# Performance work log

Hardware: AMD Instinct MI355X
Metric: run time of the kernel (lower is better)

The kernel has to match this reference:

```python
import jax, jax.numpy as jnp
import numpy as np

B, L, D_IN, D_MODEL, D_STATE, N_LAYERS = 16, 2048, 64, 512, 16, 4
LN_EPS = 1e-5


def setup_inputs() -> dict:
    key = jax.random.key(0)
    ks = jax.random.split(key, 16)
    s = 0.02
    x = jax.random.normal(ks[0], (B, L, D_IN), jnp.float32)
    W_in0 = jax.random.normal(ks[1], (D_IN, D_MODEL), jnp.float32) * s
    b_in0 = jnp.zeros((D_MODEL,), jnp.float32)
    W_in = jax.random.normal(ks[2], (N_LAYERS - 1, D_MODEL, D_MODEL), jnp.float32) * s
    b_in = jnp.zeros((N_LAYERS - 1, D_MODEL), jnp.float32)
    # S4D-style init: A_log = log(1..N) per channel
    A_log = jnp.broadcast_to(jnp.log(jnp.arange(1, D_STATE + 1, dtype=jnp.float32)), (N_LAYERS, D_MODEL, D_STATE)).copy()
    D_skip = jnp.ones((N_LAYERS, D_MODEL), jnp.float32)
    W_dt = jax.random.normal(ks[3], (N_LAYERS, D_MODEL, D_MODEL), jnp.float32) * s
    b_dt = jnp.full((N_LAYERS, D_MODEL), -4.0, jnp.float32)  # small initial dt
    W_B = jax.random.normal(ks[4], (N_LAYERS, D_MODEL, D_STATE), jnp.float32) * s
    W_C = jax.random.normal(ks[5], (N_LAYERS, D_MODEL, D_STATE), jnp.float32) * s
    ln_g = jnp.ones((D_MODEL,), jnp.float32)
    ln_b = jnp.zeros((D_MODEL,), jnp.float32)
    head_w = jax.random.normal(ks[6], (D_MODEL, 1), jnp.float32) * s
    head_b = jnp.zeros((1,), jnp.float32)
    return {"x": x, "W_in0": W_in0, "b_in0": b_in0, "W_in": W_in, "b_in": b_in,
            "A_log": A_log, "D_skip": D_skip, "W_dt": W_dt, "b_dt": b_dt,
            "W_B": W_B, "W_C": W_C, "ln_g": ln_g, "ln_b": ln_b,
            "head_w": head_w, "head_b": head_b}


def _mamba_layer(x, W_in_l, b_in_l, A_log_l, D_l, W_dt_l, b_dt_l, W_B_l, W_C_l):
    # x: (B, L, d_in) -> y: (B, L, D_MODEL)
    u = x @ W_in_l + b_in_l                    # (B, L, D)
    dt = jax.nn.softplus(u @ W_dt_l + b_dt_l)  # (B, L, D)
    Bm = u @ W_B_l                             # (B, L, N)
    Cm = u @ W_C_l                             # (B, L, N)
    A = -jnp.exp(A_log_l)                      # (D, N)

    def step(h, inp):
        dt_t, u_t, B_t, C_t = inp              # (B,D),(B,D),(B,N),(B,N)
        dA = jnp.exp(dt_t[..., None] * A)      # (B, D, N)
        h = dA * h + (dt_t * u_t)[..., None] * B_t[:, None, :]
        y_t = jnp.einsum('bdn,bn->bd', h, C_t)
        return h, y_t

    h0 = jnp.zeros((u.shape[0], u.shape[2], A.shape[1]), u.dtype)
    xs = (jnp.swapaxes(dt, 0, 1), jnp.swapaxes(u, 0, 1),
          jnp.swapaxes(Bm, 0, 1), jnp.swapaxes(Cm, 0, 1))
    _, ys = jax.lax.scan(step, h0, xs)         # ys: (L, B, D)
    return jnp.swapaxes(ys, 0, 1) + u * D_l


def reference(x, W_in0, b_in0, W_in, b_in, A_log, D_skip, W_dt, b_dt, W_B, W_C, ln_g, ln_b, head_w, head_b):
    h = x
    for i in range(N_LAYERS):
        Wi = W_in0 if i == 0 else W_in[i - 1]
        bi = b_in0 if i == 0 else b_in[i - 1]
        h = _mamba_layer(h, Wi, bi, A_log[i], D_skip[i], W_dt[i], b_dt[i], W_B[i], W_C[i])
    # LayerNorm over d_model
    mu = jnp.mean(h, axis=-1, keepdims=True)
    var = jnp.mean(jnp.square(h - mu), axis=-1, keepdims=True)
    h = (h - mu) * jax.lax.rsqrt(var + LN_EPS) * ln_g + ln_b
    return h[:, -1, :] @ head_w + head_b       # (B, 1)
```

## Files before the change

kernel.cpp:

```cpp
#include <hip/hip_runtime.h>
#include <hip/hip_bf16.h>
#include <cstdint>
#include <cstddef>

#define B_SZ    16
#define L_SZ    2048
#define DIN     64
#define DMODEL  512
#define DSTATE  16
#define NLAYERS 4
#define LN_EPS  1e-5f
#define NC      32
#define TCH     (L_SZ / NC)
#define NFUSED  (2 * DMODEL)

typedef __bf16 bf16x8 __attribute__((ext_vector_type(8)));
typedef float  f32x4  __attribute__((ext_vector_type(4)));
typedef unsigned short u16;
typedef unsigned int   u32;

__device__ __forceinline__ u16 f2bf(float f) {
    u32 u = __builtin_bit_cast(u32, f);
    u += 0x7fffu + ((u >> 16) & 1u);
    return (u16)(u >> 16);
}
__device__ __forceinline__ float bf2f(u16 v) {
    u32 u = ((u32)v) << 16;
    return __builtin_bit_cast(float, u);
}

__device__ __forceinline__ void pow16(float q, float* a_) {
    float q2 = q * q, q4 = q2 * q2, q8 = q4 * q4;
    a_[0] = q;        a_[1] = q2;       a_[2] = q2 * q;   a_[3] = q4;
    a_[4] = q4 * q;   a_[5] = q4 * q2;  a_[6] = a_[5] * q; a_[7] = q8;
    a_[8] = q8 * q;   a_[9] = q8 * q2;  a_[10] = a_[9] * q; a_[11] = q8 * q4;
    a_[12] = a_[11] * q; a_[13] = a_[11] * q2; a_[14] = a_[13] * q; a_[15] = q8 * q8;
}

#define LOG2E 1.4426950408889634f

__device__ __forceinline__ void gload16(const void* g, void* l) {
    __builtin_amdgcn_global_load_lds(
        (__attribute__((address_space(1))) void*)(g),
        (__attribute__((address_space(3))) void*)(l), 16, 0, 0);
}

template <int K>
__global__ __launch_bounds__(512) void gemm_fused(
    const u16* __restrict__ A, const u16* __restrict__ BT,
    const float* __restrict__ bias, u16* __restrict__ Cu,
    u16* __restrict__ Cdt, int M)
{
    constexpr int BM = 128, BK = 32;
    constexpr int NT = K / BK;
    __shared__ u16 As[2][BM * BK];
    __shared__ u16 Bs[2][BM * BK];

    const int tid = threadIdx.x;
    const int wv = tid >> 6, ln = tid & 63;
    const int mb = blockIdx.x & 255, nb = blockIdx.x >> 8;
    const int bm = mb * BM, bn = nb * BM;
    const int wm = (wv >> 1) * 32, wn = (wv & 1) * 64;

    f32x4 acc[2][4];
#pragma unroll
    for (int i = 0; i < 2; ++i)
#pragma unroll
        for (int j = 0; j < 4; ++j) acc[i][j] = (f32x4){0.f, 0.f, 0.f, 0.f};

    const int sm = tid >> 2, ss = tid & 3;
    const int ksrc = (ss ^ ((sm >> 1) & 3)) * 8;
    auto stage = [&](int buf, int k0) {
        gload16(A + (size_t)(bm + sm) * K + k0 + ksrc, &As[buf][(wv * 64) * 8]);
        gload16(BT + (size_t)(bn + sm) * K + k0 + ksrc, &Bs[buf][(wv * 64) * 8]);
    };

    stage(0, 0);
    if (NT > 1) stage(1, BK);

#pragma unroll
    for (int kt = 0; kt < NT; ++kt) {
        if (kt == NT - 1) asm volatile("s_waitcnt vmcnt(0)" ::: "memory");
        else              asm volatile("s_waitcnt vmcnt(2)" ::: "memory");
        __builtin_amdgcn_s_barrier();

        const int buf = kt & 1;
        const int g = ln >> 4, lm = ln & 15;
        bf16x8 af[2], bfr[4];
#pragma unroll
        for (int e = 0; e < 2; ++e) {
            int ml = wm + e * 16 + lm;
            af[e] = *(const bf16x8*)&As[buf][ml * 32 + ((g ^ ((ml >> 1) & 3)) * 8)];
        }
#pragma unroll
        for (int f = 0; f < 4; ++f) {
            int nl = wn + f * 16 + lm;
            bfr[f] = *(const bf16x8*)&Bs[buf][nl * 32 + ((g ^ ((nl >> 1) & 3)) * 8)];
        }
#pragma unroll
        for (int e = 0; e < 2; ++e)
#pragma unroll
            for (int f = 0; f < 4; ++f)
                acc[e][f] = __builtin_amdgcn_mfma_f32_16x16x32_bf16(
                    af[e], bfr[f], acc[e][f], 0, 0, 0);

        asm volatile("s_waitcnt lgkmcnt(0)" ::: "memory");
        __builtin_amdgcn_s_barrier();
        if (kt + 2 < NT) stage(buf, (kt + 2) * BK);
    }

    const int cg = ln >> 4, lc = ln & 15;
    const bool uside = (bn < DMODEL);
#pragma unroll
    for (int e = 0; e < 2; ++e) {
#pragma unroll
        for (int f = 0; f < 4; ++f) {
            int col = bn + wn + f * 16 + lc;
            float bv = bias[col];
#pragma unroll
            for (int r = 0; r < 4; ++r) {
                int row = bm + wm + e * 16 + cg * 4 + r;
                float v = acc[e][f][r] + bv;
                if (uside) {
                    Cu[(size_t)row * DMODEL + col] = f2bf(v);
                } else {
                    v = (v > 20.f) ? v : __logf(1.f + __expf(v));
                    Cdt[(size_t)row * DMODEL + (col - DMODEL)] = f2bf(v);
                }
            }
        }
    }
}

__global__ __launch_bounds__(256) void wtrans(
    const float* __restrict__ W, u16* __restrict__ WT, int K, int N,
    size_t inStride, size_t outStride)
{
    __shared__ float tile[32][33];
    const float* Wm = W + (size_t)blockIdx.z * inStride;
    u16* WTm = WT + (size_t)blockIdx.z * outStride;
    int k0 = blockIdx.x * 32, n0 = blockIdx.y * 32;
    int tx = threadIdx.x & 31, ty = threadIdx.x >> 5;
#pragma unroll
    for (int i = 0; i < 4; ++i)
        tile[ty + 8 * i][tx] = Wm[(size_t)(k0 + ty + 8 * i) * N + n0 + tx];
    __syncthreads();
#pragma unroll
    for (int i = 0; i < 4; ++i)
        WTm[(size_t)(n0 + ty + 8 * i) * K + k0 + tx] = f2bf(tile[tx][ty + 8 * i]);
}

__global__ __launch_bounds__(256) void wcombo(
    const float* __restrict__ Win, const float* __restrict__ Wdt,
    u16* __restrict__ outT, int KD,
    size_t winStride, size_t wdtStride, size_t outStride)
{
    __shared__ float wi[16][516];
    __shared__ float wd[512][16];
    const float* WinL = Win + (size_t)blockIdx.z * winStride;
    const float* WdtL = Wdt + (size_t)blockIdx.z * wdtStride;
    u16* outL = outT + (size_t)blockIdx.z * outStride;
    const int k0 = blockIdx.x * 16, n0 = blockIdx.y * 16;
    const int tid = threadIdx.x;
    for (int i = tid; i < 16 * 128; i += 256) {
        int r = i >> 7, c = i & 127;
        *(float4*)&wi[r][c * 4] =
            *(const float4*)&WinL[(size_t)(k0 + r) * DMODEL + c * 4];
    }
    for (int i = tid; i < 512 * 4; i += 256) {
        int j = i >> 2, c = i & 3;
        *(float4*)&wd[j][c * 4] =
            *(const float4*)&WdtL[(size_t)j * DMODEL + n0 + c * 4];
    }
    __syncthreads();
    const int kk = tid & 15, nn = tid >> 4;
    float acc = 0.f;
#pragma unroll 8
    for (int j = 0; j < 512; ++j)
        acc = fmaf(wi[kk][j], wd[j][nn], acc);
    outL[(size_t)(n0 + nn) * KD + k0 + kk] = f2bf(acc);
}

__global__ __launch_bounds__(256) void biasprep(
    const float* __restrict__ bin, const float* __restrict__ Wdt,
    const float* __restrict__ bdt, float* __restrict__ biascat,
    size_t binStride, size_t wdtStride, size_t bdtStride, size_t outStride)
{
    const float* binL = bin + (size_t)blockIdx.z * binStride;
    const float* WdtL = Wdt + (size_t)blockIdx.z * wdtStride;
    const float* bdtL = bdt + (size_t)blockIdx.z * bdtStride;
    float* outL = biascat + (size_t)blockIdx.z * outStride;
    int idx = blockIdx.x * 256 + threadIdx.x;
    if (idx < DMODEL) { outL[idx] = binL[idx]; return; }
    int n = idx - DMODEL;
    float acc = bdtL[n];
    for (int j = 0; j < DMODEL; ++j)
        acc = fmaf(binL[j], WdtL[(size_t)j * DMODEL + n], acc);
    outL[idx] = acc;
}

__global__ __launch_bounds__(256) void castx(
    const float* __restrict__ x, u16* __restrict__ xb, int n4)
{
    int i = blockIdx.x * 256 + threadIdx.x;
    if (i < n4) {
        float4 v = ((const float4*)x)[i];
        ushort4 o;
        o.x = f2bf(v.x); o.y = f2bf(v.y); o.z = f2bf(v.z); o.w = f2bf(v.w);
        ((ushort4*)xb)[i] = o;
    }
}

__global__ __launch_bounds__(256) void prep_wbc(
    const float* __restrict__ WB, const float* __restrict__ WC,
    u16* __restrict__ WBCT)
{
    int idx = blockIdx.x * 256 + threadIdx.x;
    int l = idx >> 14;
    int r = idx & 16383;
    int n = r >> 9, k = r & 511;
    float v = (n < 16) ? WB[((size_t)l * DMODEL + k) * DSTATE + n]
                       : WC[((size_t)l * DMODEL + k) * DSTATE + (n - 16)];
    WBCT[((size_t)l * 32 + n) * DMODEL + k] = f2bf(v);
}

__global__ __launch_bounds__(256) void gemm_bc_mfma(
    const u16* __restrict__ A, const u16* __restrict__ WBCT,
    float* __restrict__ Bo, float* __restrict__ Co)
{
    const int tid = threadIdx.x;
    const int wv = tid >> 6, ln = tid & 63;
    const int m0 = blockIdx.x * 64 + wv * 16;
    const int g = ln >> 4, lm = ln & 15;

    f32x4 accB = (f32x4){0.f, 0.f, 0.f, 0.f};
    f32x4 accC = (f32x4){0.f, 0.f, 0.f, 0.f};
    const u16* arow = A + (size_t)(m0 + lm) * DMODEL;
    const u16* wb = WBCT + (size_t)lm * DMODEL;
    const u16* wc = WBCT + (size_t)(lm + 16) * DMODEL;
#pragma unroll
    for (int ks = 0; ks < DMODEL / 32; ++ks) {
        int ko = ks * 32 + g * 8;
        bf16x8 a = *(const bf16x8*)&arow[ko];
        bf16x8 b = *(const bf16x8*)&wb[ko];
        bf16x8 c = *(const bf16x8*)&wc[ko];
        accB = __builtin_amdgcn_mfma_f32_16x16x32_bf16(a, b, accB, 0, 0, 0);
        accC = __builtin_amdgcn_mfma_f32_16x16x32_bf16(a, c, accC, 0, 0, 0);
    }
#pragma unroll
    for (int r = 0; r < 4; ++r) {
        int m = m0 + g * 4 + r;
        Bo[(size_t)m * DSTATE + lm] = accB[r];
        Co[(size_t)m * DSTATE + lm] = accC[r];
    }
}

__global__ __launch_bounds__(256) void scan_pass1(
    const u16* __restrict__ u, const u16* __restrict__ dt,
    const float* __restrict__ Bm, const float* __restrict__ A_log,
    float* __restrict__ P, float* __restrict__ S)
{
    const int tid = threadIdx.x;
    const int d = blockIdx.x * 256 + tid;
    const int c = blockIdx.y, b = blockIdx.z;
    __shared__ float Bs[TCH][DSTATE];

    const float* Bsrc = Bm + ((size_t)b * L_SZ + (size_t)c * TCH) * DSTATE;
    for (int i = tid; i < TCH * DSTATE / 4; i += 256)
        ((float4*)Bs)[i] = ((const float4*)Bsrc)[i];

    float Ac[16];
#pragma unroll
    for (int n = 0; n < 16; ++n) Ac[n] = -__expf(A_log[d * DSTATE + n]);
    bool geo = true;
#pragma unroll
    for (int n = 1; n < 16; ++n)
        geo &= fabsf(Ac[n] - (n + 1) * Ac[0]) <= 1e-4f * (n + 1) * fabsf(Ac[0]);
    __syncthreads();

    float s[16];
#pragma unroll
    for (int n = 0; n < 16; ++n) s[n] = 0.f;

    const size_t base = ((size_t)b * L_SZ + (size_t)c * TCH) * DMODEL + d;
    size_t o = (((size_t)b * NC + c) * DMODEL + d) * DSTATE;

    if (geo) {
        const float cK = Ac[0] * LOG2E;
        float qp = 1.f;
#pragma unroll 2
        for (int t = 0; t < TCH; ++t) {
            float dtv = bf2f(dt[base + (size_t)t * DMODEL]);
            float uv  = bf2f(u [base + (size_t)t * DMODEL]);
            float du = dtv * uv;
            float q = exp2f(dtv * cK);
            qp *= q;
            float a_[16];
            pow16(q, a_);
#pragma unroll
            for (int n = 0; n < 16; ++n)
                s[n] = fmaf(a_[n], s[n], du * Bs[t][n]);
        }
        float p_[16];
        pow16(qp, p_);
#pragma unroll
        for (int n = 0; n < 16; ++n) { P[o + n] = p_[n]; S[o + n] = s[n]; }
    } else {
        float p[16];
#pragma unroll
        for (int n = 0; n < 16; ++n) p[n] = 1.f;
#pragma unroll 2
        for (int t = 0; t < TCH; ++t) {
            float dtv = bf2f(dt[base + (size_t)t * DMODEL]);
            float uv  = bf2f(u [base + (size_t)t * DMODEL]);
            float du = dtv * uv;
#pragma unroll
            for (int n = 0; n < 16; ++n) {
                float a = __expf(dtv * Ac[n]);
                p[n] *= a;
                s[n] = fmaf(a, s[n], du * Bs[t][n]);
            }
        }
#pragma unroll
        for (int n = 0; n < 16; ++n) { P[o + n] = p[n]; S[o + n] = s[n]; }
    }
}

__global__ __launch_bounds__(256) void scan_fix(
    const float* __restrict__ P, const float* __restrict__ S,
    float* __restrict__ H0)
{
    const int idx = blockIdx.x * 256 + threadIdx.x;
    const int dn = idx & (DMODEL * DSTATE - 1);
    const int b = idx >> 13;
    float h = 0.f;
#pragma unroll
    for (int c = 0; c < NC; ++c) {
        size_t o = (((size_t)b * NC + c) << 13) + dn;
        H0[o] = h;
        h = fmaf(P[o], h, S[o]);
    }
}

__global__ __launch_bounds__(256) void scan_pass2(
    const u16* __restrict__ u, const u16* __restrict__ dt,
    const float* __restrict__ Bm, const float* __restrict__ Cm,
    const float* __restrict__ A_log, const float* __restrict__ Dskip,
    const float* __restrict__ H0, u16* __restrict__ yb,
    float* __restrict__ ylast)
{
    const int tid = threadIdx.x;
    const int d = blockIdx.x * 256 + tid;
    const int c = blockIdx.y, b = blockIdx.z;
    __shared__ float Bs[TCH][DSTATE];
    __shared__ float Cs[TCH][DSTATE];

    const float* Bsrc = Bm + ((size_t)b * L_SZ + (size_t)c * TCH) * DSTATE;
    const float* Csrc = Cm + ((size_t)b * L_SZ + (size_t)c * TCH) * DSTATE;
    for (int i = tid; i < TCH * DSTATE / 4; i += 256) {
        ((float4*)Bs)[i] = ((const float4*)Bsrc)[i];
        ((float4*)Cs)[i] = ((const float4*)Csrc)[i];
    }

    float Ac[16];
#pragma unroll
    for (int n = 0; n < 16; ++n) Ac[n] = -__expf(A_log[d * DSTATE + n]);
    bool geo = true;
#pragma unroll
    for (int n = 1; n < 16; ++n)
        geo &= fabsf(Ac[n] - (n + 1) * Ac[0]) <= 1e-4f * (n + 1) * fabsf(Ac[0]);
    const float Dk = Dskip[d];

    float h[16];
    size_t ho = (((size_t)b * NC + c) * DMODEL + d) * DSTATE;
#pragma unroll
    for (int n = 0; n < 16; ++n) h[n] = H0[ho + n];
    __syncthreads();

    const size_t base = ((size_t)b * L_SZ + (size_t)c * TCH) * DMODEL + d;

    if (geo) {
        const float cK = Ac[0] * LOG2E;
#pragma unroll 2
        for (int t = 0; t < TCH; ++t) {
            float dtv = bf2f(dt[base + (size_t)t * DMODEL]);
            float uv  = bf2f(u [base + (size_t)t * DMODEL]);
            float du = dtv * uv;
            float q = exp2f(dtv * cK);
            float a_[16];
            pow16(q, a_);
            float yv = 0.f;
#pragma unroll
            for (int n = 0; n < 16; ++n) {
                h[n] = fmaf(a_[n], h[n], du * Bs[t][n]);
                yv = fmaf(h[n], Cs[t][n], yv);
            }
            yv = fmaf(uv, Dk, yv);
            yb[base + (size_t)t * DMODEL] = f2bf(yv);
            if (c == NC - 1 && t == TCH - 1) ylast[(size_t)b * DMODEL + d] = yv;
        }
    } else {
#pragma unroll 2
        for (int t = 0; t < TCH; ++t) {
            float dtv = bf2f(dt[base + (size_t)t * DMODEL]);
            float uv  = bf2f(u [base + (size_t)t * DMODEL]);
            float du = dtv * uv;
            float yv = 0.f;
#pragma unroll
            for (int n = 0; n < 16; ++n) {
                float a = __expf(dtv * Ac[n]);
                h[n] = fmaf(a, h[n], du * Bs[t][n]);
                yv = fmaf(h[n], Cs[t][n], yv);
            }
            yv = fmaf(uv, Dk, yv);
            yb[base + (size_t)t * DMODEL] = f2bf(yv);
            if (c == NC - 1 && t == TCH - 1) ylast[(size_t)b * DMODEL + d] = yv;
        }
    }
}

__global__ __launch_bounds__(256) void ln_head_kernel(
    const float* __restrict__ ylast, const float* __restrict__ g,
    const float* __restrict__ bb, const float* __restrict__ hw,
    const float* __restrict__ hb, float* __restrict__ out)
{
    const int b = blockIdx.x;
    const int tid = threadIdx.x;
    const float* row = ylast + (size_t)b * DMODEL;
    float v0 = row[tid], v1 = row[tid + 256];
    float s = v0 + v1;
    float s2 = v0 * v0 + v1 * v1;
#pragma unroll
    for (int o = 32; o >= 1; o >>= 1) {
        s += __shfl_xor(s, o);
        s2 += __shfl_xor(s2, o);
    }
    __shared__ float red[8];
    const int w = tid >> 6;
    if ((tid & 63) == 0) { red[w] = s; red[4 + w] = s2; }
    __syncthreads();
    s = red[0] + red[1] + red[2] + red[3];
    s2 = red[4] + red[5] + red[6] + red[7];
    float mu = s * (1.f / DMODEL);
    float var = s2 * (1.f / DMODEL) - mu * mu;
    float r = rsqrtf(var + LN_EPS);
    float c = ((v0 - mu) * r * g[tid] + bb[tid]) * hw[tid]
            + ((v1 - mu) * r * g[tid + 256] + bb[tid + 256]) * hw[tid + 256];
#pragma unroll
    for (int o = 32; o >= 1; o >>= 1) c += __shfl_xor(c, o);
    __syncthreads();
    if ((tid & 63) == 0) red[w] = c;
    __syncthreads();
    if (tid == 0) out[b] = red[0] + red[1] + red[2] + red[3] + hb[0];
}

extern "C" void kernel_launch(void* const* d_in, const int* in_sizes, int n_in,
                              void* d_out, int out_size, void* d_ws, size_t ws_size,
                              hipStream_t stream)
{
    const float* x      = (const float*)d_in[0];
    const float* W_in0  = (const float*)d_in[1];
    const float* b_in0  = (const float*)d_in[2];
    const float* W_in   = (const float*)d_in[3];
    const float* b_in   = (const float*)d_in[4];
    const float* A_log  = (const float*)d_in[5];
    const float* D_skip = (const float*)d_in[6];
    const float* W_dt   = (const float*)d_in[7];
    const float* b_dt   = (const float*)d_in[8];
    const float* W_B    = (const float*)d_in[9];
    const float* W_C    = (const float*)d_in[10];
    const float* ln_g   = (const float*)d_in[11];
    const float* ln_b   = (const float*)d_in[12];
    const float* head_w = (const float*)d_in[13];
    const float* head_b = (const float*)d_in[14];
    float* out = (float*)d_out;

    const size_t BLD = (size_t)B_SZ * L_SZ * DMODEL;
    const size_t BLN = (size_t)B_SZ * L_SZ * DSTATE;
    const size_t BCD = (size_t)B_SZ * NC * DMODEL * DSTATE;
    const size_t XBN = (size_t)B_SZ * L_SZ * DIN;

    float* fp = (float*)d_ws;
    float* Bbuf  = fp; fp += BLN;
    float* Cbuf  = fp; fp += BLN;
    float* Pbuf  = fp; fp += BCD;
    float* Sbuf  = fp; fp += BCD;
    float* H0buf = fp; fp += BCD;
    float* ylast = fp; fp += (size_t)B_SZ * DMODEL;
    float* biascat = fp; fp += (size_t)NLAYERS * NFUSED;
    u16* hp = (u16*)fp;
    u16* xb    = hp; hp += XBN;
    u16* ub    = hp; hp += BLD;
    u16* dtb   = hp; hp += BLD;
    u16* ybuf  = hp; hp += BLD;
    u16* BT0   = hp; hp += (size_t)NFUSED * DIN;
    u16* BTcat = hp; hp += (size_t)(NLAYERS - 1) * NFUSED * DMODEL;
    u16* WBCT  = hp; hp += (size_t)NLAYERS * 32 * DMODEL;

    const int M = B_SZ * L_SZ;

    castx<<<(XBN / 4 + 255) / 256, 256, 0, stream>>>(x, xb, XBN / 4);
    prep_wbc<<<(NLAYERS * 32 * DMODEL) / 256, 256, 0, stream>>>(W_B, W_C, WBCT);
    wtrans<<<dim3(DIN / 32, DMODEL / 32, 1), 256, 0, stream>>>(
        W_in0, BT0, DIN, DMODEL, 0, 0);
    wcombo<<<dim3(DIN / 16, DMODEL / 16, 1), 256, 0, stream>>>(
        W_in0, W_dt, BT0 + (size_t)DMODEL * DIN, DIN, 0, 0, 0);
    biasprep<<<dim3(4, 1, 1), 256, 0, stream>>>(
        b_in0, W_dt, b_dt, biascat, 0, 0, 0, 0);
    wtrans<<<dim3(DMODEL / 32, DMODEL / 32, NLAYERS - 1), 256, 0, stream>>>(
        W_in, BTcat, DMODEL, DMODEL,
        (size_t)DMODEL * DMODEL, (size_t)NFUSED * DMODEL);
    wcombo<<<dim3(DMODEL / 16, DMODEL / 16, NLAYERS - 1), 256, 0, stream>>>(
        W_in, W_dt + (size_t)DMODEL * DMODEL,
        BTcat + (size_t)DMODEL * DMODEL, DMODEL,
        (size_t)DMODEL * DMODEL, (size_t)DMODEL * DMODEL,
        (size_t)NFUSED * DMODEL);
    biasprep<<<dim3(4, 1, NLAYERS - 1), 256, 0, stream>>>(
        b_in, W_dt + (size_t)DMODEL * DMODEL, b_dt + DMODEL, biascat + NFUSED,
        DMODEL, (size_t)DMODEL * DMODEL, DMODEL, NFUSED);

    for (int l = 0; l < NLAYERS; ++l) {
        if (l == 0) {
            gemm_fused<DIN><<<(M / 128) * (NFUSED / 128), 512, 0, stream>>>(
                xb, BT0, biascat, ub, dtb, M);
        } else {
            gemm_fused<DMODEL><<<(M / 128) * (NFUSED / 128), 512, 0, stream>>>(
                ybuf, BTcat + (size_t)(l - 1) * NFUSED * DMODEL,
                biascat + (size_t)l * NFUSED, ub, dtb, M);
        }
        gemm_bc_mfma<<<M / 64, 256, 0, stream>>>(
            ub, WBCT + (size_t)l * 32 * DMODEL, Bbuf, Cbuf);
        const float* Al = A_log + (size_t)l * DMODEL * DSTATE;
        scan_pass1<<<dim3(DMODEL / 256, NC, B_SZ), 256, 0, stream>>>(
            ub, dtb, Bbuf, Al, Pbuf, Sbuf);
        scan_fix<<<(B_SZ * DMODEL * DSTATE) / 256, 256, 0, stream>>>(
            Pbuf, Sbuf, H0buf);
        scan_pass2<<<dim3(DMODEL / 256, NC, B_SZ), 256, 0, stream>>>(
            ub, dtb, Bbuf, Cbuf, Al, D_skip + (size_t)l * DMODEL,
            H0buf, ybuf, ylast);
    }

    ln_head_kernel<<<B_SZ, 256, 0, stream>>>(ylast, ln_g, ln_b, head_w, head_b, out);
}
```

Baseline: 691.7 us.

## Deepen GEMM LDS pipeline to four stages and store compact chunk decay

The fused GEMM moves from two to four LDS buffers with a three-tile prefetch distance. This removes the second barrier and lgkmcnt wait in each k-step, and it raises wave priority around the MFMA block. Separately, scan_pass1 on the geometric-A path writes one scalar chunk decay per channel instead of 16 powers. scan_fix rebuilds each power by repeated squaring, which cuts P-buffer write and read traffic. In exchange the GEMM uses twice the shared memory, which may lower occupancy, and the single-barrier scheme depends on four buffers keeping the reuse of each buffer safe.

```diff
diff --git a/kernel.cpp b/kernel.cpp
--- a/kernel.cpp
+++ b/kernel.cpp
@@ -53,8 +53,8 @@
 {
     constexpr int BM = 128, BK = 32;
     constexpr int NT = K / BK;
-    __shared__ u16 As[2][BM * BK];
-    __shared__ u16 Bs[2][BM * BK];
+    __shared__ u16 As[4][BM * BK];
+    __shared__ u16 Bs[4][BM * BK];
 
     const int tid = threadIdx.x;
     const int wv = tid >> 6, ln = tid & 63;
@@ -71,20 +71,24 @@
     const int sm = tid >> 2, ss = tid & 3;
     const int ksrc = (ss ^ ((sm >> 1) & 3)) * 8;
     auto stage = [&](int buf, int k0) {
-        gload16(A + (size_t)(bm + sm) * K + k0 + ksrc, &As[buf][(wv * 64) * 8]);
-        gload16(BT + (size_t)(bn + sm) * K + k0 + ksrc, &Bs[buf][(wv * 64) * 8]);
+        gload16(A + (size_t)(bm + sm) * K + k0 + ksrc, &As[buf][wv * 512]);
+        gload16(BT + (size_t)(bn + sm) * K + k0 + ksrc, &Bs[buf][wv * 512]);
     };
 
     stage(0, 0);
     if (NT > 1) stage(1, BK);
+    if (NT > 2) stage(2, 2 * BK);
 
 #pragma unroll
     for (int kt = 0; kt < NT; ++kt) {
-        if (kt == NT - 1) asm volatile("s_waitcnt vmcnt(0)" ::: "memory");
-        else              asm volatile("s_waitcnt vmcnt(2)" ::: "memory");
+        if (kt == NT - 1)      asm volatile("s_waitcnt vmcnt(0)" ::: "memory");
+        else if (kt == NT - 2) asm volatile("s_waitcnt vmcnt(2)" ::: "memory");
+        else                   asm volatile("s_waitcnt vmcnt(4)" ::: "memory");
         __builtin_amdgcn_s_barrier();
 
-        const int buf = kt & 1;
+        if (kt + 3 < NT) stage((kt + 3) & 3, (kt + 3) * BK);
+
+        const int buf = kt & 3;
         const int g = ln >> 4, lm = ln & 15;
         bf16x8 af[2], bfr[4];
 #pragma unroll
@@ -97,16 +101,14 @@
             int nl = wn + f * 16 + lm;
             bfr[f] = *(const bf16x8*)&Bs[buf][nl * 32 + ((g ^ ((nl >> 1) & 3)) * 8)];
         }
+        __builtin_amdgcn_s_setprio(1);
 #pragma unroll
         for (int e = 0; e < 2; ++e)
 #pragma unroll
             for (int f = 0; f < 4; ++f)
                 acc[e][f] = __builtin_amdgcn_mfma_f32_16x16x32_bf16(
                     af[e], bfr[f], acc[e][f], 0, 0, 0);
-
-        asm volatile("s_waitcnt lgkmcnt(0)" ::: "memory");
-        __builtin_amdgcn_s_barrier();
-        if (kt + 2 < NT) stage(buf, (kt + 2) * BK);
+        __builtin_amdgcn_s_setprio(0);
     }
 
     const int cg = ln >> 4, lc = ln & 15;
@@ -258,7 +260,7 @@
 __global__ __launch_bounds__(256) void scan_pass1(
     const u16* __restrict__ u, const u16* __restrict__ dt,
     const float* __restrict__ Bm, const float* __restrict__ A_log,
-    float* __restrict__ P, float* __restrict__ S)
+    float* __restrict__ P, float* __restrict__ S, float* __restrict__ Q)
 {
     const int tid = threadIdx.x;
     const int d = blockIdx.x * 256 + tid;
@@ -301,10 +303,9 @@
             for (int n = 0; n < 16; ++n)
                 s[n] = fmaf(a_[n], s[n], du * Bs[t][n]);
         }
-        float p_[16];
-        pow16(qp, p_);
-#pragma unroll
-        for (int n = 0; n < 16; ++n) { P[o + n] = p_[n]; S[o + n] = s[n]; }
+        Q[((size_t)b * NC + c) * DMODEL + d] = qp;
+#pragma unroll
+        for (int n = 0; n < 16; ++n) S[o + n] = s[n];
     } else {
         float p[16];
 #pragma unroll
@@ -328,17 +329,42 @@
 
 __global__ __launch_bounds__(256) void scan_fix(
     const float* __restrict__ P, const float* __restrict__ S,
+    const float* __restrict__ Q, const float* __restrict__ A_log,
     float* __restrict__ H0)
 {
     const int idx = blockIdx.x * 256 + threadIdx.x;
     const int dn = idx & (DMODEL * DSTATE - 1);
     const int b = idx >> 13;
+    const int d = dn >> 4, n = dn & 15;
+
+    float Ac0 = -__expf(A_log[d * DSTATE + 0]);
+    bool geo = true;
+#pragma unroll
+    for (int j = 1; j < 16; ++j) {
+        float Acj = -__expf(A_log[d * DSTATE + j]);
+        geo &= fabsf(Acj - (j + 1) * Ac0) <= 1e-4f * (j + 1) * fabsf(Ac0);
+    }
+
     float h = 0.f;
 #pragma unroll
     for (int c = 0; c < NC; ++c) {
         size_t o = (((size_t)b * NC + c) << 13) + dn;
         H0[o] = h;
-        h = fmaf(P[o], h, S[o]);
+        float p;
+        if (geo) {
+            float base = Q[((size_t)b * NC + c) * DMODEL + d];
+            p = 1.f;
+            int e = n + 1;
+#pragma unroll
+            for (int i = 0; i < 5; ++i) {
+                if (e & 1) p *= base;
+                base *= base;
+                e >>= 1;
+            }
+        } else {
+            p = P[o];
+        }
+        h = fmaf(p, h, S[o]);
     }
 }
 
@@ -478,6 +504,7 @@
     const size_t BLD = (size_t)B_SZ * L_SZ * DMODEL;
     const size_t BLN = (size_t)B_SZ * L_SZ * DSTATE;
     const size_t BCD = (size_t)B_SZ * NC * DMODEL * DSTATE;
+    const size_t BCDQ = (size_t)B_SZ * NC * DMODEL;
     const size_t XBN = (size_t)B_SZ * L_SZ * DIN;
 
     float* fp = (float*)d_ws;
@@ -486,6 +513,7 @@
     float* Pbuf  = fp; fp += BCD;
     float* Sbuf  = fp; fp += BCD;
     float* H0buf = fp; fp += BCD;
+    float* Qbuf  = fp; fp += BCDQ;
     float* ylast = fp; fp += (size_t)B_SZ * DMODEL;
     float* biascat = fp; fp += (size_t)NLAYERS * NFUSED;
     u16* hp = (u16*)fp;
@@ -532,9 +560,9 @@
             ub, WBCT + (size_t)l * 32 * DMODEL, Bbuf, Cbuf);
         const float* Al = A_log + (size_t)l * DMODEL * DSTATE;
         scan_pass1<<<dim3(DMODEL / 256, NC, B_SZ), 256, 0, stream>>>(
-            ub, dtb, Bbuf, Al, Pbuf, Sbuf);
+            ub, dtb, Bbuf, Al, Pbuf, Sbuf, Qbuf);
         scan_fix<<<(B_SZ * DMODEL * DSTATE) / 256, 256, 0, stream>>>(
-            Pbuf, Sbuf, H0buf);
+            Pbuf, Sbuf, Qbuf, Al, H0buf);
         scan_pass2<<<dim3(DMODEL / 256, NC, B_SZ), 256, 0, stream>>>(
             ub, dtb, Bbuf, Cbuf, Al, D_skip + (size_t)l * DMODEL,
             H0buf, ybuf, ylast);
```

New measurement: 747.7 us. +8.1%, slower.
